# Optimization experiments

Measured on AMD Instinct MI355X. Metric: run time of the kernel, lower is better.

## Reference

```python
import jax, jax.numpy as jnp
import numpy as np
import math

PHI = (1.0 + math.sqrt(5.0)) / 2.0
V, D, L, N, H = 50257, 128, 2, 512, 8
DH = D // H
B, S = 2, 256


def setup_inputs() -> dict:
    key = jax.random.key(0)
    ks = jax.random.split(key, 16)
    lim = 0.5 * math.sqrt(6.0 / (N + D))  # xavier_uniform gain=0.5 for Linear(N->D)
    return {
        "tokens": jax.random.randint(ks[0], (B, S), 0, V),
        "emb": (jax.random.normal(ks[1], (V, 2 * D)) * 0.02) * 0.5,
        "wq": jax.random.normal(ks[2], (L, H, DH)) * 0.02,
        "bq": jnp.zeros((L, H, DH)),
        "wk": jax.random.normal(ks[3], (L, H, DH)) * 0.02,
        "bk": jnp.zeros((L, H, DH)),
        "w_out": jax.random.normal(ks[4], (L, D)) * 0.02,
        "b_out": jnp.zeros((L, D)),
        "out_scale": jnp.ones((L, D)) * 0.5,
        "Wf": jax.random.normal(ks[5], (L, N, D)) * 0.02,
        "Bf": jnp.zeros((L, N, D)),
        "proj_real": jax.random.uniform(ks[6], (L, D, N), minval=-lim, maxval=lim),
        "proj_imag": jax.random.uniform(ks[7], (L, D, N), minval=-lim, maxval=lim),
        "attn_scale": jnp.ones((L,)),
        "res_scale": jnp.ones((L,)),
        "out_proj": jax.random.normal(ks[8], (V, D)) * 0.02,
    }


def reference(tokens, emb, wq, bq, wk, bk, w_out, b_out, out_scale, Wf, Bf,
              proj_real, proj_imag, attn_scale, res_scale, out_proj):
    dtype = emb.dtype
    wb = emb[tokens]                      # [B,S,2D] token -> (w, b) pairs
    w_e, b_e = wb[..., :D], wb[..., D:]
    t = jnp.arange(S, dtype=dtype)        # timestep per position

    # Recurrent Euler state evolution: theta = s/(1+|w|) + b + t*PHI ; s' = cos+sin
    def step(s, inp):
        w_t, b_t, tt = inp
        theta = s / (1.0 + jnp.abs(w_t)) + b_t + tt * PHI
        s_new = jnp.cos(theta) + jnp.sin(theta)
        return s_new, s_new

    _, states = jax.lax.scan(
        step, jnp.zeros((B, D), dtype),
        (jnp.moveaxis(w_e, 1, 0), jnp.moveaxis(b_e, 1, 0), t))
    states = jnp.moveaxis(states, 0, 1)   # [B,S,D] cached states

    causal = jnp.tril(jnp.ones((S, S), bool))  # cache includes current state
    t_phi = t * PHI
    scale = math.sqrt(2 * DH)

    x = states
    for l in range(L):
        # --- Euler attention ---
        xh = x.reshape(B, S, H, DH)
        th_q = xh / (1.0 + jnp.abs(wq[l])) + bq[l] + t_phi[None, :, None, None]
        q = jnp.concatenate([jnp.cos(th_q), jnp.sin(th_q)], axis=-1)  # [B,S,H,2DH]
        kh = states.reshape(B, S, H, DH)
        th_k = kh / (1.0 + jnp.abs(wk[l])) + bk[l]
        k = jnp.concatenate([jnp.cos(th_k), jnp.sin(th_k)], axis=-1)
        scores = jnp.einsum('bqhd,bkhd->bhqk', q, k) / scale
        scores = jnp.where(causal[None, None], scores, -jnp.inf)
        wts = jax.nn.softmax(scores, axis=-1)
        # each head attends over full-width cached states; heads are summed
        context = jnp.einsum('bhqk,bkd->bqd', wts, states)
        th_o = context / (1.0 + jnp.abs(w_out[l])) + b_out[l] + t_phi[None, :, None]
        attn_out = out_scale[l] * (jnp.cos(th_o) + jnp.sin(th_o))
        # --- Resonant FFN (per-neuron interference) ---
        th_f = x[:, :, None, :] / (1.0 + jnp.abs(Wf[l])) + Bf[l] + t[None, :, None, None]
        cos_sum = jnp.cos(th_f).sum(axis=-1)   # [B,S,N]
        sin_sum = jnp.sin(th_f).sum(axis=-1)
        res = cos_sum @ proj_real[l].T + sin_sum @ proj_imag[l].T
        res = jax.nn.silu(res)
        # additive fusion
        x = x + attn_scale[l] * attn_out + res_scale[l] * res

    logits = x @ out_proj.T                # [B,S,V]
    return logits
```

## Files before the change

### kernel.cpp

```cpp
#include <hip/hip_runtime.h>
#include <hip/hip_bf16.h>

using bf16x8 = __attribute__((ext_vector_type(8))) short;
using f32x4  = __attribute__((ext_vector_type(4))) float;

constexpr int cV  = 50257;
constexpr int cVp = 50304;
constexpr int cD  = 128;
constexpr int cN  = 512;
constexpr int cS  = 256;

#define PHI_F    1.6180339887498949f
#define INV2PI_F 0.15915494309189535f
#define SQRT2_F  1.4142135623730951f

__device__ __forceinline__ float fract1(float x) { return x - floorf(x); }

#if __has_builtin(__builtin_amdgcn_sinf)
__device__ __forceinline__ float sin_rev(float r) { return __builtin_amdgcn_sinf(r); }
__device__ __forceinline__ float cos_rev(float r) { return __builtin_amdgcn_cosf(r); }
#else
__device__ __forceinline__ float sin_rev(float r) { return __sinf(r * 6.2831853071795865f); }
__device__ __forceinline__ float cos_rev(float r) { return __cosf(r * 6.2831853071795865f); }
#endif

__device__ __forceinline__ unsigned short f2bf(float f) {
  unsigned u = __float_as_uint(f);
  unsigned r = (u + 0x7FFFu + ((u >> 16) & 1u)) >> 16;
  return (unsigned short)r;
}

__global__ void k_setup(const int* __restrict__ tokens, const float* __restrict__ emb,
                        float2* __restrict__ mc,
                        const float* __restrict__ pr, const float* __restrict__ pi,
                        float* __restrict__ pTR, float* __restrict__ pTI,
                        const float* __restrict__ W, unsigned short* __restrict__ Wbf) {
  int blk = blockIdx.x;
  if (blk < 256) {
    int idx = blk * 256 + threadIdx.x;
    int t = idx & 255, s = idx >> 8;
    int b = t >> 7, d = t & 127;
    int tok = tokens[b * cS + s];
    float w  = emb[tok * (2 * cD) + d];
    float be = emb[tok * (2 * cD) + cD + d];
    float m2 = SQRT2_F * INV2PI_F / (1.f + fabsf(w));
    float c  = fmaf((float)s, PHI_F, be) * INV2PI_F + 0.125f;
    mc[idx] = make_float2(m2, c);
  } else if (blk < 768) {
    int idx = (blk - 256) * 256 + threadIdx.x;
    int l = idx >> 16, rem = idx & 65535;
    int n = rem >> 7, d = rem & 127;
    int src = (l * cD + d) * cN + n;
    pTR[idx] = pr[src];
    pTI[idx] = pi[src];
  } else {
    int idx = (blk - 768) * 256 + threadIdx.x;
    int row = idx >> 4, c0 = (idx & 15) * 8;
    ushort4 o0 = {0,0,0,0}, o1 = {0,0,0,0};
    if (row < cV) {
      float4 w0 = *(const float4*)(W + (size_t)row * cD + c0);
      float4 w1 = *(const float4*)(W + (size_t)row * cD + c0 + 4);
      o0 = { f2bf(w0.x), f2bf(w0.y), f2bf(w0.z), f2bf(w0.w) };
      o1 = { f2bf(w1.x), f2bf(w1.y), f2bf(w1.z), f2bf(w1.w) };
    }
    unsigned short* dst = Wbf + (size_t)row * cD + c0;
    *(ushort4*)dst = o0;
    *(ushort4*)(dst + 4) = o1;
  }
}

__global__ void k_scan(const float2* __restrict__ mc, float* __restrict__ states) {
  int t = threadIdx.x;
  int b = t >> 7, d = t & 127;
  float2 buf[8];
#pragma unroll
  for (int i = 0; i < 8; ++i) buf[i] = mc[i * 256 + t];
  float sv = 0.f;
  float* out = states + (b * cS) * cD + d;
#pragma unroll 8
  for (int s = 0; s < cS; ++s) {
    float2 v = buf[s & 7];
    if (s + 8 < cS) buf[s & 7] = mc[(s + 8) * 256 + t];
    float r = fmaf(sv, v.x, v.y);
    sv = sin_rev(fract1(r));
    out[s * cD] = sv * SQRT2_F;
  }
}

__global__ __launch_bounds__(512) void k_layer(const float* __restrict__ x, const float* __restrict__ states,
                                               const float* __restrict__ wq, const float* __restrict__ bq,
                                               const float* __restrict__ wk, const float* __restrict__ bk,
                                               const float* __restrict__ Wf, const float* __restrict__ Bf,
                                               float* __restrict__ ctx, float* __restrict__ U, float* __restrict__ Vv) {
  int blk = blockIdx.x;
  if (blk < 256) {
    __shared__ __align__(16) float qrow[2][256];
    __shared__ float Psum[2][256];
    __shared__ float redm[2][4], reds[2][4];
    __shared__ float cred[2][256];
    __shared__ __align__(16) float rkl[128], bkl[128];
    int b = blk >> 7, qp = blk & 127;
    int sub = threadIdx.x >> 8;
    int t = threadIdx.x & 255;
    int q = qp * 2 + sub;
    if (threadIdx.x < 128) {
      int hd = threadIdx.x;
      rkl[hd] = INV2PI_F / (1.f + fabsf(wk[hd]));
      bkl[hd] = bk[hd] * INV2PI_F;
    }
    if (t < 128) {
      int hd = t;
      float rq = 1.f / (1.f + fabsf(wq[hd]));
      float thq = fmaf(x[(b * cS + q) * cD + hd], rq, fmaf((float)q, PHI_F, bq[hd])) * INV2PI_F;
      float fq = fract1(thq);
      qrow[sub][hd]       = cos_rev(fq);
      qrow[sub][128 + hd] = sin_rev(fq);
    }
    Psum[sub][t] = 0.f;
    __syncthreads();
    bool act = (t <= q);
    float sc[8];
    const float4* Sr = (const float4*)(states + (b * cS + t) * cD);
#pragma unroll
    for (int h = 0; h < 8; ++h) {
      float sacc = 0.f;
#pragma unroll
      for (int j = 0; j < 4; ++j) {
        float4 sv4 = Sr[h * 4 + j];
        int hd = h * 16 + j * 4;
        float sva[4] = { sv4.x, sv4.y, sv4.z, sv4.w };
#pragma unroll
        for (int c = 0; c < 4; ++c) {
          float f = fract1(fmaf(sva[c], rkl[hd + c], bkl[hd + c]));
          float ck = cos_rev(f), sk = sin_rev(f);
          sacc = fmaf(qrow[sub][hd + c], ck, fmaf(qrow[sub][128 + hd + c], sk, sacc));
        }
      }
      sc[h] = act ? sacc * 0.17677669529663689f : -3.0e38f;
    }
    int wid = t >> 6;
    for (int h = 0; h < 8; ++h) {
      float v = sc[h];
#pragma unroll
      for (int off = 32; off; off >>= 1) v = fmaxf(v, __shfl_xor(v, off, 64));
      if ((t & 63) == 0) redm[sub][wid] = v;
      __syncthreads();
      float m = fmaxf(fmaxf(redm[sub][0], redm[sub][1]), fmaxf(redm[sub][2], redm[sub][3]));
      float p = act ? __expf(sc[h] - m) : 0.f;
      float ps = p;
#pragma unroll
      for (int off = 32; off; off >>= 1) ps += __shfl_xor(ps, off, 64);
      if ((t & 63) == 0) reds[sub][wid] = ps;
      __syncthreads();
      float tot = reds[sub][0] + reds[sub][1] + reds[sub][2] + reds[sub][3];
      Psum[sub][t] += p / tot;
    }
    __syncthreads();
    int d = t & 127, half = t >> 7;
    float acc = 0.f;
    int k0 = half * 128;
    int kend = min(k0 + 128, q + 1);
    for (int kk = k0; kk < kend; ++kk)
      acc = fmaf(Psum[sub][kk], states[(b * cS + kk) * cD + d], acc);
    cred[sub][t] = acc;
    __syncthreads();
    if (half == 0) ctx[(b * cS + q) * cD + d] = cred[sub][t] + cred[sub][t + 128];
  } else {
    int fblk = blk - 256;
    int ns = fblk & 15, tg = fblk >> 4;
    constexpr int P = 130;
    __shared__ __align__(16) float finv[32 * P];
    __shared__ __align__(16) float fb[32 * P];
    __shared__ __align__(16) float xl[32 * 128];
    int t = threadIdx.x;
#pragma unroll
    for (int i = 0; i < 8; ++i) {
      int idx = t + i * 512;
      int rl = idx >> 7, d = idx & 127;
      int g = (ns * 32 + rl) * cD + d;
      finv[rl * P + d] = INV2PI_F / (1.f + fabsf(Wf[g]));
      fb[rl * P + d]   = Bf[g] * INV2PI_F;
      xl[idx] = x[(tg * 32 + rl) * cD + d];
    }
    __syncthreads();
    int nl = t & 31, tli = t >> 5;
#pragma unroll
    for (int p = 0; p < 2; ++p) {
      int tl = p * 16 + tli;
      int T = tg * 32 + tl;
      float srev = (float)(T & 255) * INV2PI_F;
      float uc = 0.f, us = 0.f;
      const float* fi  = finv + nl * P;
      const float* fbp = fb + nl * P;
      const float* xr  = xl + tl * 128;
#pragma unroll 4
      for (int d = 0; d < cD; d += 2) {
        float2 fiv = *(const float2*)(fi + d);
        float2 fbv = *(const float2*)(fbp + d);
        float2 xv  = *(const float2*)(xr + d);
        float f0 = fract1(fmaf(xv.x, fiv.x, fbv.x) + srev);
        float f1 = fract1(fmaf(xv.y, fiv.y, fbv.y) + srev);
        uc += cos_rev(f0);
        us += sin_rev(f0);
        uc += cos_rev(f1);
        us += sin_rev(f1);
      }
      U[T * cN + ns * 32 + nl]  = uc;
      Vv[T * cN + ns * 32 + nl] = us;
    }
  }
}

__global__ __launch_bounds__(256) void k_res(const float* __restrict__ U, const float* __restrict__ Vv,
                                             const float* __restrict__ pTR, const float* __restrict__ pTI,
                                             const float* __restrict__ ctx, const float* __restrict__ x,
                                             const float* __restrict__ w_out, const float* __restrict__ b_out,
                                             const float* __restrict__ out_scale,
                                             const float* __restrict__ attn_scale, const float* __restrict__ res_scale,
                                             int l, float* __restrict__ xout, unsigned short* __restrict__ xbf) {
  int T = blockIdx.x;
  int t = threadIdx.x;
  __shared__ __align__(16) float uvU[512], uvV[512];
  __shared__ __align__(16) float4 part[8][32];
  uvU[t]       = U[T * cN + t];
  uvU[t + 256] = U[T * cN + 256 + t];
  uvV[t]       = Vv[T * cN + t];
  uvV[t + 256] = Vv[T * cN + 256 + t];
  __syncthreads();
  int d4 = t & 31, nh = t >> 5;
  float a0 = 0.f, a1 = 0.f, a2 = 0.f, a3 = 0.f;
  const float* prB = pTR + (size_t)(l * cN) * cD + d4 * 4;
  const float* piB = pTI + (size_t)(l * cN) * cD + d4 * 4;
  int n0 = nh * 64;
#pragma unroll 4
  for (int n = n0; n < n0 + 64; ++n) {
    float4 pr = *(const float4*)(prB + n * cD);
    float4 pi = *(const float4*)(piB + n * cD);
    float wr = uvU[n], wi = uvV[n];
    a0 = fmaf(wr, pr.x, fmaf(wi, pi.x, a0));
    a1 = fmaf(wr, pr.y, fmaf(wi, pi.y, a1));
    a2 = fmaf(wr, pr.z, fmaf(wi, pi.z, a2));
    a3 = fmaf(wr, pr.w, fmaf(wi, pi.w, a3));
  }
  if (nh > 0) part[nh][d4] = make_float4(a0, a1, a2, a3);
  __syncthreads();
  if (nh == 0) {
    float rr[4] = { a0, a1, a2, a3 };
#pragma unroll
    for (int j = 1; j < 8; ++j) {
      float4 p = part[j][d4];
      rr[0] += p.x; rr[1] += p.y; rr[2] += p.z; rr[3] += p.w;
    }
    int s = T & 255;
    int di = d4 * 4;
    float4 cx  = *(const float4*)(ctx + T * cD + di);
    float4 wo  = *(const float4*)(w_out + l * cD + di);
    float4 bo  = *(const float4*)(b_out + l * cD + di);
    float4 osc = *(const float4*)(out_scale + l * cD + di);
    float4 xv  = *(const float4*)(x + T * cD + di);
    float as = attn_scale[l], rs = res_scale[l];
    float sphi = (float)s * PHI_F;
    float cxa[4] = { cx.x, cx.y, cx.z, cx.w };
    float woa[4] = { wo.x, wo.y, wo.z, wo.w };
    float boa[4] = { bo.x, bo.y, bo.z, bo.w };
    float osa[4] = { osc.x, osc.y, osc.z, osc.w };
    float xva[4] = { xv.x, xv.y, xv.z, xv.w };
    float oa[4];
#pragma unroll
    for (int c = 0; c < 4; ++c) {
      float th = fmaf(cxa[c], 1.f / (1.f + fabsf(woa[c])), boa[c]) + sphi;
      float f = fract1(th * INV2PI_F);
      float ao = osa[c] * (cos_rev(f) + sin_rev(f));
      float r = rr[c];
      float sil = r / (1.f + __expf(-r));
      oa[c] = fmaf(as, ao, fmaf(rs, sil, xva[c]));
    }
    *(float4*)(xout + T * cD + di) = make_float4(oa[0], oa[1], oa[2], oa[3]);
    if (xbf) {
      ushort4 b4 = { f2bf(oa[0]), f2bf(oa[1]), f2bf(oa[2]), f2bf(oa[3]) };
      *(ushort4*)(xbf + T * cD + di) = b4;
    }
  }
}

__global__ __launch_bounds__(512, 4) void k_gemm(const unsigned short* __restrict__ Xbf,
                                                 const unsigned short* __restrict__ Wbf,
                                                 float* __restrict__ out) {
  __shared__ __align__(16) float Cw[8][16 * 36];
  int t = threadIdx.x, bid = blockIdx.x;
  int v0 = (bid >> 1) * 64, m0 = (bid & 1) * 256;
  int wid = t >> 6, lane = t & 63, lr = lane & 15, lk = lane >> 4;
  int wm = (wid >> 1) * 64, wv = (wid & 1) * 32;
  const bf16x8* Xp = (const bf16x8*)Xbf;
  const bf16x8* Wp = (const bf16x8*)Wbf;
  bf16x8 b[4][2];
#pragma unroll
  for (int ks = 0; ks < 4; ++ks)
#pragma unroll
    for (int fv = 0; fv < 2; ++fv)
      b[ks][fv] = Wp[(size_t)(v0 + wv + fv * 16 + lr) * 16 + ks * 4 + lk];
  bf16x8 aCur[4], aNxt[4];
#pragma unroll
  for (int fm = 0; fm < 4; ++fm)
    aCur[fm] = Xp[(m0 + wm + fm * 16 + lr) * 16 + lk];
  f32x4 acc[4][2];
#pragma unroll
  for (int fm = 0; fm < 4; ++fm)
#pragma unroll
    for (int fv = 0; fv < 2; ++fv) acc[fm][fv] = (f32x4){0.f, 0.f, 0.f, 0.f};
#pragma unroll
  for (int ks = 0; ks < 4; ++ks) {
    if (ks < 3) {
#pragma unroll
      for (int fm = 0; fm < 4; ++fm)
        aNxt[fm] = Xp[(m0 + wm + fm * 16 + lr) * 16 + (ks + 1) * 4 + lk];
    }
#pragma unroll
    for (int fm = 0; fm < 4; ++fm)
#pragma unroll
      for (int fv = 0; fv < 2; ++fv)
        acc[fm][fv] = __builtin_amdgcn_mfma_f32_16x16x32_bf16(aCur[fm], b[ks][fv], acc[fm][fv], 0, 0, 0);
#pragma unroll
    for (int fm = 0; fm < 4; ++fm) aCur[fm] = aNxt[fm];
  }
  float* Cp = &Cw[wid][0];
  int rowl = lane >> 2, cg = lane & 3;
#pragma unroll
  for (int fm = 0; fm < 4; ++fm) {
#pragma unroll
    for (int fv = 0; fv < 2; ++fv)
#pragma unroll
      for (int r = 0; r < 4; ++r)
        Cp[(lk * 4 + r) * 36 + fv * 16 + lr] = acc[fm][fv][r];
    float4 c0 = *(const float4*)&Cp[rowl * 36 + cg * 4];
    float4 c1 = *(const float4*)&Cp[rowl * 36 + 16 + cg * 4];
    size_t rb = (size_t)(m0 + wm + fm * 16 + rowl) * cV;
    int cb0 = v0 + wv + cg * 4;
    int cb1 = cb0 + 16;
    if (cb1 + 3 < cV) {
      *(float4*)(out + rb + cb0) = c0;
      *(float4*)(out + rb + cb1) = c1;
    } else {
      float ca0[4] = { c0.x, c0.y, c0.z, c0.w };
      float ca1[4] = { c1.x, c1.y, c1.z, c1.w };
#pragma unroll
      for (int j = 0; j < 4; ++j) {
        if (cb0 + j < cV) out[rb + cb0 + j] = ca0[j];
        if (cb1 + j < cV) out[rb + cb1 + j] = ca1[j];
      }
    }
  }
}

extern "C" void kernel_launch(void* const* d_in, const int* in_sizes, int n_in,
                              void* d_out, int out_size, void* d_ws, size_t ws_size,
                              hipStream_t stream) {
  const int*   tokens    = (const int*)d_in[0];
  const float* emb       = (const float*)d_in[1];
  const float* wq        = (const float*)d_in[2];
  const float* bq        = (const float*)d_in[3];
  const float* wk        = (const float*)d_in[4];
  const float* bk        = (const float*)d_in[5];
  const float* w_out     = (const float*)d_in[6];
  const float* b_out     = (const float*)d_in[7];
  const float* out_scale = (const float*)d_in[8];
  const float* Wf        = (const float*)d_in[9];
  const float* Bf        = (const float*)d_in[10];
  const float* pr        = (const float*)d_in[11];
  const float* pi        = (const float*)d_in[12];
  const float* attn_s    = (const float*)d_in[13];
  const float* res_s     = (const float*)d_in[14];
  const float* out_proj  = (const float*)d_in[15];
  float* out = (float*)d_out;
  float* ws  = (float*)d_ws;

  float*  states = ws;
  float*  x1     = ws + 65536;
  float*  x2     = ws + 131072;
  float*  ctx    = ws + 196608;
  float2* mc     = (float2*)(ws + 262144);
  float*  U      = ws + 393216;
  float*  Vv     = ws + 655360;
  float*  pTR    = ws + 917504;
  float*  pTI    = ws + 1048576;
  unsigned short* X2bf = (unsigned short*)(ws + 1179648);
  unsigned short* Wbf  = (unsigned short*)(ws + 1212416);

  k_setup<<<768 + (cVp * 16) / 256, 256, 0, stream>>>(tokens, emb, mc, pr, pi, pTR, pTI,
                                                      out_proj, Wbf);
  k_scan<<<1, 256, 0, stream>>>(mc, states);

  const float* xin = states;
  float* xouts[2] = { x1, x2 };
  for (int l = 0; l < 2; ++l) {
    k_layer<<<512, 512, 0, stream>>>(xin, states, wq + l * 128, bq + l * 128,
                                     wk + l * 128, bk + l * 128,
                                     Wf + l * 65536, Bf + l * 65536, ctx, U, Vv);
    k_res<<<512, 256, 0, stream>>>(U, Vv, pTR, pTI, ctx, xin, w_out, b_out, out_scale,
                                   attn_s, res_s, l, xouts[l],
                                   (l == 1) ? X2bf : (unsigned short*)nullptr);
    xin = xouts[l];
  }
  k_gemm<<<1572, 512, 0, stream>>>(X2bf, Wbf, out);
}
```

Before: 179.7 us.

## Retile logits GEMM to 256-column vocab tiles covering all rows

```diff
diff --git a/kernel.cpp b/kernel.cpp
--- a/kernel.cpp
+++ b/kernel.cpp
@@ -5,7 +5,7 @@
 using f32x4  = __attribute__((ext_vector_type(4))) float;
 
 constexpr int cV  = 50257;
-constexpr int cVp = 50304;
+constexpr int cVp = 50432;
 constexpr int cD  = 128;
 constexpr int cN  = 512;
 constexpr int cS  = 256;
@@ -283,70 +283,41 @@
   }
 }
 
-__global__ __launch_bounds__(512, 4) void k_gemm(const unsigned short* __restrict__ Xbf,
-                                                 const unsigned short* __restrict__ Wbf,
-                                                 float* __restrict__ out) {
-  __shared__ __align__(16) float Cw[8][16 * 36];
-  int t = threadIdx.x, bid = blockIdx.x;
-  int v0 = (bid >> 1) * 64, m0 = (bid & 1) * 256;
+__global__ __launch_bounds__(1024) void k_gemm(const unsigned short* __restrict__ Xbf,
+                                               const unsigned short* __restrict__ Wbf,
+                                               float* __restrict__ out) {
+  int t = threadIdx.x;
+  int v0 = blockIdx.x * 256;
   int wid = t >> 6, lane = t & 63, lr = lane & 15, lk = lane >> 4;
-  int wm = (wid >> 1) * 64, wv = (wid & 1) * 32;
+  int wm = wid * 32;
   const bf16x8* Xp = (const bf16x8*)Xbf;
   const bf16x8* Wp = (const bf16x8*)Wbf;
-  bf16x8 b[4][2];
-#pragma unroll
-  for (int ks = 0; ks < 4; ++ks)
-#pragma unroll
-    for (int fv = 0; fv < 2; ++fv)
-      b[ks][fv] = Wp[(size_t)(v0 + wv + fv * 16 + lr) * 16 + ks * 4 + lk];
-  bf16x8 aCur[4], aNxt[4];
-#pragma unroll
-  for (int fm = 0; fm < 4; ++fm)
-    aCur[fm] = Xp[(m0 + wm + fm * 16 + lr) * 16 + lk];
-  f32x4 acc[4][2];
-#pragma unroll
-  for (int fm = 0; fm < 4; ++fm)
-#pragma unroll
-    for (int fv = 0; fv < 2; ++fv) acc[fm][fv] = (f32x4){0.f, 0.f, 0.f, 0.f};
+  f32x4 acc[2][16];
+#pragma unroll
+  for (int fm = 0; fm < 2; ++fm)
+#pragma unroll
+    for (int fv = 0; fv < 16; ++fv) acc[fm][fv] = (f32x4){0.f, 0.f, 0.f, 0.f};
 #pragma unroll
   for (int ks = 0; ks < 4; ++ks) {
-    if (ks < 3) {
-#pragma unroll
-      for (int fm = 0; fm < 4; ++fm)
-        aNxt[fm] = Xp[(m0 + wm + fm * 16 + lr) * 16 + (ks + 1) * 4 + lk];
-    }
-#pragma unroll
-    for (int fm = 0; fm < 4; ++fm)
-#pragma unroll
-      for (int fv = 0; fv < 2; ++fv)
-        acc[fm][fv] = __builtin_amdgcn_mfma_f32_16x16x32_bf16(aCur[fm], b[ks][fv], acc[fm][fv], 0, 0, 0);
-#pragma unroll
-    for (int fm = 0; fm < 4; ++fm) aCur[fm] = aNxt[fm];
-  }
-  float* Cp = &Cw[wid][0];
-  int rowl = lane >> 2, cg = lane & 3;
-#pragma unroll
-  for (int fm = 0; fm < 4; ++fm) {
-#pragma unroll
-    for (int fv = 0; fv < 2; ++fv)
-#pragma unroll
-      for (int r = 0; r < 4; ++r)
-        Cp[(lk * 4 + r) * 36 + fv * 16 + lr] = acc[fm][fv][r];
-    float4 c0 = *(const float4*)&Cp[rowl * 36 + cg * 4];
-    float4 c1 = *(const float4*)&Cp[rowl * 36 + 16 + cg * 4];
-    size_t rb = (size_t)(m0 + wm + fm * 16 + rowl) * cV;
-    int cb0 = v0 + wv + cg * 4;
-    int cb1 = cb0 + 16;
-    if (cb1 + 3 < cV) {
-      *(float4*)(out + rb + cb0) = c0;
-      *(float4*)(out + rb + cb1) = c1;
-    } else {
-      float ca0[4] = { c0.x, c0.y, c0.z, c0.w };
-      float ca1[4] = { c1.x, c1.y, c1.z, c1.w };
-#pragma unroll
-      for (int j = 0; j < 4; ++j) {
-        if (cb0 + j < cV) out[rb + cb0 + j] = ca0[j];
-        if (cb1 + j < cV) out[rb + cb1 + j] = ca1[j];
+    bf16x8 a0 = Xp[(wm + lr) * 16 + ks * 4 + lk];
+    bf16x8 a1 = Xp[(wm + 16 + lr) * 16 + ks * 4 + lk];
+#pragma unroll
+    for (int fv = 0; fv < 16; ++fv) {
+      bf16x8 b = Wp[(size_t)(v0 + fv * 16 + lr) * 16 + ks * 4 + lk];
+      acc[0][fv] = __builtin_amdgcn_mfma_f32_16x16x32_bf16(a0, b, acc[0][fv], 0, 0, 0);
+      acc[1][fv] = __builtin_amdgcn_mfma_f32_16x16x32_bf16(a1, b, acc[1][fv], 0, 0, 0);
+    }
+  }
+#pragma unroll
+  for (int fm = 0; fm < 2; ++fm) {
+    size_t rbase = (size_t)(wm + fm * 16 + lk * 4) * cV;
+#pragma unroll
+    for (int fv = 0; fv < 16; ++fv) {
+      int col = v0 + fv * 16 + lr;
+      if (col < cV) {
+#pragma unroll
+        for (int r = 0; r < 4; ++r)
+          out[rbase + (size_t)r * cV + col] = acc[fm][fv][r];
       }
     }
   }
@@ -401,5 +372,5 @@
                                    (l == 1) ? X2bf : (unsigned short*)nullptr);
     xin = xouts[l];
   }
-  k_gemm<<<1572, 512, 0, stream>>>(X2bf, Wbf, out);
-}
+  k_gemm<<<(cV + 255) / 256, 1024, 0, stream>>>(X2bf, Wbf, out);
+}
```

Measured after the change: 247.8 us. +37.9%, slower.
